# Optimization experiments

Measured on AMD Instinct MI355X. Metric: run time of the kernel, lower is better.

## Reference

```python
import jax, jax.numpy as jnp
import numpy as np

DIM = 768
NUM_HEADS = 16
D_K = DIM // NUM_HEADS


def setup_inputs() -> dict:
    key = jax.random.key(0)
    ks = jax.random.split(key, 9)
    B, T = 4, 2048
    s = 1.0 / np.sqrt(DIM)
    return {
        "x": jax.random.normal(ks[0], (B, T, DIM), dtype=jnp.float32),
        "Wq": jax.random.normal(ks[1], (DIM, DIM), dtype=jnp.float32) * s,
        "bq": jnp.zeros((DIM,), dtype=jnp.float32),
        "Wk": jax.random.normal(ks[2], (DIM, DIM), dtype=jnp.float32) * s,
        "bk": jnp.zeros((DIM,), dtype=jnp.float32),
        "Wv": jax.random.normal(ks[3], (DIM, DIM), dtype=jnp.float32) * s,
        "bv": jnp.zeros((DIM,), dtype=jnp.float32),
        "Wp": jax.random.normal(ks[4], (DIM, DIM), dtype=jnp.float32) * s,
        "bp": jnp.zeros((DIM,), dtype=jnp.float32),
    }


def reference(x, Wq, bq, Wk, bk, Wv, bv, Wp, bp):
    B, T, _ = x.shape
    # QKV projections (weights stored as [in, out])
    q = x @ Wq + bq
    k = x @ Wk + bk
    v = x @ Wv + bv
    # split heads: (B, H, T, d_k)
    q = q.reshape(B, T, NUM_HEADS, D_K).transpose(0, 2, 1, 3)
    k = k.reshape(B, T, NUM_HEADS, D_K).transpose(0, 2, 1, 3)
    v = v.reshape(B, T, NUM_HEADS, D_K).transpose(0, 2, 1, 3)
    # scaled dot-product attention; dropout omitted (eval mode)
    scores = jnp.einsum("bhtd,bhsd->bhts", q, k) / jnp.sqrt(jnp.float32(D_K))
    attn = jax.nn.softmax(scores, axis=-1)
    out = jnp.einsum("bhts,bhsd->bhtd", attn, v)
    out = out.transpose(0, 2, 1, 3).reshape(B, T, DIM)
    return out @ Wp + bp
```

## Files before the change

kernel.cpp:

```cpp
#include <hip/hip_runtime.h>
#include <math.h>

#define T_SEQ 2048
#define B_SZ  4
#define DIM   768
#define NH    16
#define DK    48
#define NQK   1536
#define N3    2304
#define LDQ   56
#define LDK   72
#define LDP   72

typedef __bf16 bf16x8 __attribute__((ext_vector_type(8)));
typedef float  f32x4  __attribute__((ext_vector_type(4)));

__device__ __forceinline__ unsigned short f32_to_bf16(float f) {
    unsigned u = __float_as_uint(f);
    u += 0x7FFFu + ((u >> 16) & 1u);
    return (unsigned short)(u >> 16);
}
__device__ __forceinline__ unsigned pack_bf16x2(float a, float b) {
    return (unsigned)f32_to_bf16(a) | ((unsigned)f32_to_bf16(b) << 16);
}
__device__ __forceinline__ void lds_dma16(const unsigned short* g, unsigned short* l) {
    __builtin_amdgcn_global_load_lds(
        (const __attribute__((address_space(1))) unsigned int*)g,
        (__attribute__((address_space(3))) unsigned int*)l, 16, 0, 0);
}

__global__ __launch_bounds__(256) void cvt_x_kernel(
    const float* __restrict__ x, unsigned short* __restrict__ xb)
{
    int i = blockIdx.x * 256 + threadIdx.x;
    const float* p = x + (size_t)i * 8;
    float4 f0 = *(const float4*)p;
    float4 f1 = *(const float4*)(p + 4);
    uint4 u;
    u.x = pack_bf16x2(f0.x, f0.y);
    u.y = pack_bf16x2(f0.z, f0.w);
    u.z = pack_bf16x2(f1.x, f1.y);
    u.w = pack_bf16x2(f1.z, f1.w);
    *(uint4*)(xb + (size_t)i * 8) = u;
}

__global__ __launch_bounds__(256) void pack_w_kernel(
    const float* __restrict__ Wq, const float* __restrict__ Wk,
    const float* __restrict__ Wv, const float* __restrict__ Wp,
    unsigned short* __restrict__ Wt, unsigned short* __restrict__ Wpt,
    float qscale)
{
    __shared__ float T[32][33];
    const int mode = blockIdx.z;
    const float* W = (mode == 0) ? Wq : (mode == 1) ? Wk : (mode == 2) ? Wv : Wp;
    const float sc = (mode == 0) ? qscale : 1.0f;
    const int k0 = blockIdx.x * 32, c0 = blockIdx.y * 32;
    const int tx = threadIdx.x & 31, ty = threadIdx.x >> 5;

#pragma unroll
    for (int r = 0; r < 4; ++r) {
        int row = ty + r * 8;
        T[row][tx] = W[(size_t)(k0 + row) * DIM + c0 + tx];
    }
    __syncthreads();
#pragma unroll
    for (int r = 0; r < 4; ++r) {
        int j   = ty + r * 8;
        int col = c0 + j;
        int k   = k0 + tx;
        unsigned short v = f32_to_bf16(T[tx][j] * sc);
        if (mode < 3) Wt[(size_t)(mode * 768 + col) * DIM + k] = v;
        else          Wpt[(size_t)col * DIM + k] = v;
    }
}

__global__ __launch_bounds__(256) void pack_bias_kernel(
    const float* __restrict__ bq, const float* __restrict__ bk,
    const float* __restrict__ bv, float* __restrict__ b3, float qscale)
{
    int n = blockIdx.x * 256 + threadIdx.x;
    if (n >= N3) return;
    float v;
    if (n < 768)       v = bq[n] * qscale;
    else if (n < 1536) v = bk[n - 768];
    else               v = bv[n - 1536];
    b3[n] = v;
}

__global__ __launch_bounds__(256, 4) void gemm_qkv_kernel(
    const unsigned short* __restrict__ A, const unsigned short* __restrict__ Bt,
    const float* __restrict__ bias, unsigned short* __restrict__ QK,
    unsigned short* __restrict__ vT)
{
    __shared__ unsigned short As[128 * 32];
    __shared__ unsigned short Bs[128 * 32];

    const int t = threadIdx.x;
    const int w = t >> 6, lane = t & 63, quad = lane >> 4, lr = lane & 15;
    const int wm = w >> 1, wn = w & 1;
    const int m0 = blockIdx.y * 128, n0 = blockIdx.x * 128;

    const int cw0 = w * 128, cw1 = w * 128 + 64;
    const int ca = cw0 + lane, cb = cw1 + lane;
    const int ra = ca >> 2, sa = (ca & 3) * 8;
    const int rb = cb >> 2, sb = (cb & 3) * 8;

    f32x4 acc[4][4] = {};

    for (int k0 = 0; k0 < DIM; k0 += 32) {
        __syncthreads();
        lds_dma16(A  + (size_t)(m0 + ra) * DIM + k0 + sa, As + cw0 * 8);
        lds_dma16(A  + (size_t)(m0 + rb) * DIM + k0 + sb, As + cw1 * 8);
        lds_dma16(Bt + (size_t)(n0 + ra) * DIM + k0 + sa, Bs + cw0 * 8);
        lds_dma16(Bt + (size_t)(n0 + rb) * DIM + k0 + sb, Bs + cw1 * 8);
        __syncthreads();

        bf16x8 af[4], bfr[4];
#pragma unroll
        for (int mt = 0; mt < 4; ++mt)
            af[mt] = *(const bf16x8*)&As[(wm * 64 + mt * 16 + lr) * 32 + quad * 8];
#pragma unroll
        for (int nt = 0; nt < 4; ++nt)
            bfr[nt] = *(const bf16x8*)&Bs[(wn * 64 + nt * 16 + lr) * 32 + quad * 8];
#pragma unroll
        for (int mt = 0; mt < 4; ++mt)
#pragma unroll
            for (int nt = 0; nt < 4; ++nt)
                acc[mt][nt] = __builtin_amdgcn_mfma_f32_16x16x32_bf16(
                    af[mt], bfr[nt], acc[mt][nt], 0, 0, 0);
    }

    if (blockIdx.x < 12) {
#pragma unroll
        for (int nt = 0; nt < 4; ++nt) {
            int col = n0 + wn * 64 + nt * 16 + lr;
            float bv = bias[col];
#pragma unroll
            for (int mt = 0; mt < 4; ++mt)
#pragma unroll
                for (int r = 0; r < 4; ++r) {
                    int row = m0 + wm * 64 + mt * 16 + quad * 4 + r;
                    QK[(size_t)row * NQK + col] = f32_to_bf16(acc[mt][nt][r] + bv);
                }
        }
    } else {
        const int bidx = m0 >> 11;
        const int ts_base = (m0 & 2047) + wm * 64;
#pragma unroll
        for (int nt = 0; nt < 4; ++nt) {
            int col = n0 + wn * 64 + nt * 16 + lr;
            int vcol = col - 1536;
            int hh = vcol / 48, cc = vcol - hh * 48;
            float bv = bias[col];
            unsigned short* dst0 = vT + ((size_t)(bidx * 16 + hh) * 48 + cc) * T_SEQ;
#pragma unroll
            for (int mt = 0; mt < 4; ++mt) {
                int ts = ts_base + mt * 16 + quad * 4;
                uint2 u;
                u.x = pack_bf16x2(acc[mt][nt][0] + bv, acc[mt][nt][1] + bv);
                u.y = pack_bf16x2(acc[mt][nt][2] + bv, acc[mt][nt][3] + bv);
                *(uint2*)(dst0 + ts) = u;
            }
        }
    }
}

__global__ __launch_bounds__(256, 4) void gemm_out_kernel(
    const unsigned short* __restrict__ A, const unsigned short* __restrict__ Bt,
    const float* __restrict__ bias, float* __restrict__ C)
{
    __shared__ unsigned short As[128 * 32];
    __shared__ unsigned short Bs[128 * 32];

    const int t = threadIdx.x;
    const int w = t >> 6, lane = t & 63, quad = lane >> 4, lr = lane & 15;
    const int wm = w >> 1, wn = w & 1;
    const int m0 = blockIdx.y * 128, n0 = blockIdx.x * 128;

    const int cw0 = w * 128, cw1 = w * 128 + 64;
    const int ca = cw0 + lane, cb = cw1 + lane;
    const int ra = ca >> 2, sa = (ca & 3) * 8;
    const int rb = cb >> 2, sb = (cb & 3) * 8;

    f32x4 acc[4][4] = {};

    for (int k0 = 0; k0 < DIM; k0 += 32) {
        __syncthreads();
        lds_dma16(A  + (size_t)(m0 + ra) * DIM + k0 + sa, As + cw0 * 8);
        lds_dma16(A  + (size_t)(m0 + rb) * DIM + k0 + sb, As + cw1 * 8);
        lds_dma16(Bt + (size_t)(n0 + ra) * DIM + k0 + sa, Bs + cw0 * 8);
        lds_dma16(Bt + (size_t)(n0 + rb) * DIM + k0 + sb, Bs + cw1 * 8);
        __syncthreads();

        bf16x8 af[4], bfr[4];
#pragma unroll
        for (int mt = 0; mt < 4; ++mt)
            af[mt] = *(const bf16x8*)&As[(wm * 64 + mt * 16 + lr) * 32 + quad * 8];
#pragma unroll
        for (int nt = 0; nt < 4; ++nt)
            bfr[nt] = *(const bf16x8*)&Bs[(wn * 64 + nt * 16 + lr) * 32 + quad * 8];
#pragma unroll
        for (int mt = 0; mt < 4; ++mt)
#pragma unroll
            for (int nt = 0; nt < 4; ++nt)
                acc[mt][nt] = __builtin_amdgcn_mfma_f32_16x16x32_bf16(
                    af[mt], bfr[nt], acc[mt][nt], 0, 0, 0);
    }

#pragma unroll
    for (int nt = 0; nt < 4; ++nt) {
        int col = n0 + wn * 64 + nt * 16 + lr;
        float bv = bias[col];
#pragma unroll
        for (int mt = 0; mt < 4; ++mt)
#pragma unroll
            for (int r = 0; r < 4; ++r) {
                int row = m0 + wm * 64 + mt * 16 + quad * 4 + r;
                C[(size_t)row * DIM + col] = acc[mt][nt][r] + bv;
            }
    }
}

__global__ __launch_bounds__(512, 6) void attn_kernel(
    const unsigned short* __restrict__ QK, const unsigned short* __restrict__ vT,
    unsigned short* __restrict__ Ob)
{
    __shared__ unsigned short smem[128 * LDQ + 64 * LDK + 64 * LDK + 8 * 16 * LDP];
    unsigned short* Qs = smem;
    unsigned short* Ks = smem + 128 * LDQ;
    unsigned short* Vt = Ks + 64 * LDK;
    unsigned short* Ps = Vt + 64 * LDK;

    const int t = threadIdx.x;
    const int w = t >> 6, lane = t & 63, quad = lane >> 4, lr = lane & 15;
    const int qt = blockIdx.x, h = blockIdx.y, b = blockIdx.z;
    const int base = b * T_SEQ, q0 = qt * 128;
    const int hq = h * DK;
    const int hk = 768 + h * DK;

    {
        int r = t / 6, c = t - r * 6;
        *(uint4*)&Qs[r * LDQ + c * 8] =
            *(const uint4*)(QK + (size_t)(base + q0 + r) * NQK + hq + c * 8);
        if (t < 256) {
            int qc2 = t + 512;
            int r2 = qc2 / 6, c2 = qc2 - r2 * 6;
            *(uint4*)&Qs[r2 * LDQ + c2 * 8] =
                *(const uint4*)(QK + (size_t)(base + q0 + r2) * NQK + hq + c2 * 8);
        }
    }
    if (t < 256) {
        int r = t >> 2, c = 48 + (t & 3) * 4;
        *(uint2*)&Ks[r * LDK + c] = make_uint2(0u, 0u);
        int vr = 48 + (t >> 4), vc = (t & 15) * 4;
        unsigned ones = (vr == 48) ? 0x3F803F80u : 0u;
        *(uint2*)&Vt[vr * LDK + vc] = make_uint2(ones, ones);
    }

    f32x4 Oacc[4] = {};
    const unsigned short* vbase = vT + (size_t)(b * 16 + h) * 48 * T_SEQ;

    for (int kt = 0; kt < T_SEQ / 64; ++kt) {
        __syncthreads();
        if (t < 384) {
            int r = t / 6, c = t - r * 6;
            *(uint4*)&Ks[r * LDK + c * 8] =
                *(const uint4*)(QK + (size_t)(base + kt * 64 + r) * NQK + hk + c * 8);
        } else {
            int vc_ = t - 384;
            int d = vc_ >> 3, ch = vc_ & 7;
            *(uint4*)&Vt[d * LDK + ch * 8] =
                *(const uint4*)(vbase + (size_t)d * T_SEQ + kt * 64 + ch * 8);
        }
        if (t < 256) {
            int vc_ = 128 + t;
            int d = vc_ >> 3, ch = vc_ & 7;
            *(uint4*)&Vt[d * LDK + ch * 8] =
                *(const uint4*)(vbase + (size_t)d * T_SEQ + kt * 64 + ch * 8);
        }
        __syncthreads();

        f32x4 S[4] = {};
        bf16x8 aQ0 = *(const bf16x8*)&Qs[(w * 16 + lr) * LDQ + quad * 8];
        bf16x8 aQ1 = *(const bf16x8*)&Qs[(w * 16 + lr) * LDQ + 32 + quad * 8];
#pragma unroll
        for (int nt = 0; nt < 4; ++nt) {
            bf16x8 b0 = *(const bf16x8*)&Ks[(nt * 16 + lr) * LDK + quad * 8];
            bf16x8 b1 = *(const bf16x8*)&Ks[(nt * 16 + lr) * LDK + 32 + quad * 8];
            S[nt] = __builtin_amdgcn_mfma_f32_16x16x32_bf16(aQ0, b0, S[nt], 0, 0, 0);
            S[nt] = __builtin_amdgcn_mfma_f32_16x16x32_bf16(aQ1, b1, S[nt], 0, 0, 0);
        }

        unsigned short* Pw = Ps + w * 16 * LDP;
#pragma unroll
        for (int nt = 0; nt < 4; ++nt)
#pragma unroll
            for (int r = 0; r < 4; ++r)
                Pw[(quad * 4 + r) * LDP + nt * 16 + lr] =
                    f32_to_bf16(__builtin_amdgcn_exp2f(S[nt][r]));

        bf16x8 aP0 = *(const bf16x8*)&Pw[lr * LDP + quad * 8];
        bf16x8 aP1 = *(const bf16x8*)&Pw[lr * LDP + 32 + quad * 8];
#pragma unroll
        for (int on = 0; on < 4; ++on) {
            bf16x8 b0 = *(const bf16x8*)&Vt[(on * 16 + lr) * LDK + quad * 8];
            bf16x8 b1 = *(const bf16x8*)&Vt[(on * 16 + lr) * LDK + 32 + quad * 8];
            Oacc[on] = __builtin_amdgcn_mfma_f32_16x16x32_bf16(aP0, b0, Oacc[on], 0, 0, 0);
            Oacc[on] = __builtin_amdgcn_mfma_f32_16x16x32_bf16(aP1, b1, Oacc[on], 0, 0, 0);
        }
    }

#pragma unroll
    for (int r = 0; r < 4; ++r) {
        float l = __shfl(Oacc[3][r], lane & 0x30);
        float inv = 1.0f / l;
        int row = base + q0 + w * 16 + quad * 4 + r;
#pragma unroll
        for (int on = 0; on < 3; ++on)
            Ob[(size_t)row * DIM + h * DK + on * 16 + lr] =
                f32_to_bf16(Oacc[on][r] * inv);
    }
}

extern "C" void kernel_launch(void* const* d_in, const int* in_sizes, int n_in,
                              void* d_out, int out_size, void* d_ws, size_t ws_size,
                              hipStream_t stream) {
    (void)in_sizes; (void)n_in; (void)out_size; (void)ws_size;

    const float* x  = (const float*)d_in[0];
    const float* Wq = (const float*)d_in[1];
    const float* bq = (const float*)d_in[2];
    const float* Wk = (const float*)d_in[3];
    const float* bk = (const float*)d_in[4];
    const float* Wv = (const float*)d_in[5];
    const float* bv = (const float*)d_in[6];
    const float* Wp = (const float*)d_in[7];
    const float* bp = (const float*)d_in[8];
    float* out = (float*)d_out;

    const size_t M = (size_t)B_SZ * T_SEQ;

    char* ws = (char*)d_ws;
    unsigned short* xb  = (unsigned short*)ws;  ws += M * DIM * 2;
    unsigned short* qk  = (unsigned short*)ws;  ws += M * NQK * 2;
    unsigned short* vT  = (unsigned short*)ws;  ws += M * DIM * 2;
    unsigned short* aob = (unsigned short*)ws;  ws += M * DIM * 2;
    unsigned short* Wt  = (unsigned short*)ws;  ws += (size_t)N3 * DIM * 2;
    unsigned short* Wpt = (unsigned short*)ws;  ws += (size_t)DIM * DIM * 2;
    float*          b3  = (float*)ws;           ws += N3 * 4;

    const float qscale = 0.14433756729740643f * 1.4426950408889634f;

    cvt_x_kernel<<<dim3((int)(M * DIM / 8 / 256)), 256, 0, stream>>>(x, xb);
    pack_w_kernel<<<dim3(DIM / 32, DIM / 32, 4), 256, 0, stream>>>(
        Wq, Wk, Wv, Wp, Wt, Wpt, qscale);
    pack_bias_kernel<<<dim3((N3 + 255) / 256), 256, 0, stream>>>(bq, bk, bv, b3, qscale);

    gemm_qkv_kernel<<<dim3(N3 / 128, (int)(M / 128)), 256, 0, stream>>>(
        xb, Wt, b3, qk, vT);

    attn_kernel<<<dim3(T_SEQ / 128, NH, B_SZ), 512, 0, stream>>>(qk, vT, aob);

    gemm_out_kernel<<<dim3(DIM / 128, (int)(M / 128)), 256, 0, stream>>>(
        aob, Wpt, bp, out);
}
```

Before: 295.9 us.

## Restructure attention to load K/V fragments directly from global, drop shared staging

The attention kernel now runs 256 threads per block, each wave owning 32 query rows. Q, K and V MFMA fragments are read straight from global memory (relying on L1/L2), so the shared-memory K/V tiles and their per-iteration barriers go away. S is computed transposed (K as A operand), and the softmax row sum is accumulated with shuffles instead of an appended ones column in V. Shared memory now holds only the per-wave P buffer. The trade is redundant global/cache traffic for K/V across waves in exchange for no block-level sync. Launch-bounds occupancy hints on the GEMMs are also relaxed.

After: 361.6 us. +22.2%, slower.

```diff
diff --git a/kernel.cpp b/kernel.cpp
--- a/kernel.cpp
+++ b/kernel.cpp
@@ -8,9 +8,7 @@
 #define DK    48
 #define NQK   1536
 #define N3    2304
-#define LDQ   56
-#define LDK   72
-#define LDP   72
+#define LDP   64
 
 typedef __bf16 bf16x8 __attribute__((ext_vector_type(8)));
 typedef float  f32x4  __attribute__((ext_vector_type(4)));
@@ -87,7 +85,7 @@
     b3[n] = v;
 }
 
-__global__ __launch_bounds__(256, 4) void gemm_qkv_kernel(
+__global__ __launch_bounds__(256) void gemm_qkv_kernel(
     const unsigned short* __restrict__ A, const unsigned short* __restrict__ Bt,
     const float* __restrict__ bias, unsigned short* __restrict__ QK,
     unsigned short* __restrict__ vT)
@@ -165,7 +163,7 @@
     }
 }
 
-__global__ __launch_bounds__(256, 4) void gemm_out_kernel(
+__global__ __launch_bounds__(256) void gemm_out_kernel(
     const unsigned short* __restrict__ A, const unsigned short* __restrict__ Bt,
     const float* __restrict__ bias, float* __restrict__ C)
 {
@@ -221,104 +219,101 @@
     }
 }
 
-__global__ __launch_bounds__(512, 6) void attn_kernel(
+__global__ __launch_bounds__(256, 4) void attn_kernel(
     const unsigned short* __restrict__ QK, const unsigned short* __restrict__ vT,
     unsigned short* __restrict__ Ob)
 {
-    __shared__ unsigned short smem[128 * LDQ + 64 * LDK + 64 * LDK + 8 * 16 * LDP];
-    unsigned short* Qs = smem;
-    unsigned short* Ks = smem + 128 * LDQ;
-    unsigned short* Vt = Ks + 64 * LDK;
-    unsigned short* Ps = Vt + 64 * LDK;
+    __shared__ unsigned short Ps[128 * LDP];
 
     const int t = threadIdx.x;
     const int w = t >> 6, lane = t & 63, quad = lane >> 4, lr = lane & 15;
     const int qt = blockIdx.x, h = blockIdx.y, b = blockIdx.z;
     const int base = b * T_SEQ, q0 = qt * 128;
-    const int hq = h * DK;
-    const int hk = 768 + h * DK;
-
-    {
-        int r = t / 6, c = t - r * 6;
-        *(uint4*)&Qs[r * LDQ + c * 8] =
-            *(const uint4*)(QK + (size_t)(base + q0 + r) * NQK + hq + c * 8);
-        if (t < 256) {
-            int qc2 = t + 512;
-            int r2 = qc2 / 6, c2 = qc2 - r2 * 6;
-            *(uint4*)&Qs[r2 * LDQ + c2 * 8] =
-                *(const uint4*)(QK + (size_t)(base + q0 + r2) * NQK + hq + c2 * 8);
-        }
-    }
-    if (t < 256) {
-        int r = t >> 2, c = 48 + (t & 3) * 4;
-        *(uint2*)&Ks[r * LDK + c] = make_uint2(0u, 0u);
-        int vr = 48 + (t >> 4), vc = (t & 15) * 4;
-        unsigned ones = (vr == 48) ? 0x3F803F80u : 0u;
-        *(uint2*)&Vt[vr * LDK + vc] = make_uint2(ones, ones);
-    }
-
-    f32x4 Oacc[4] = {};
-    const unsigned short* vbase = vT + (size_t)(b * 16 + h) * 48 * T_SEQ;
+    const int hq = h * DK, hk = 768 + h * DK;
+    const int qrow = base + q0 + w * 32;
+
+    bf16x8 qa[2], qb[2];
+#pragma unroll
+    for (int mt = 0; mt < 2; ++mt) {
+        const unsigned short* qp = QK + (size_t)(qrow + mt * 16 + lr) * NQK + hq;
+        qa[mt] = *(const bf16x8*)(qp + quad * 8);
+        qb[mt] = *(const bf16x8*)(qp + 32 + quad * 8);
+    }
+
+    f32x4 Oacc[2][3] = {};
+    float l_acc[2] = {0.0f, 0.0f};
+    const unsigned short* vbase = vT + (size_t)(b * NH + h) * DK * T_SEQ;
+    unsigned short* Pw = Ps + (w * 32) * LDP;
+    const bf16x8 zfrag = {};
 
     for (int kt = 0; kt < T_SEQ / 64; ++kt) {
-        __syncthreads();
-        if (t < 384) {
-            int r = t / 6, c = t - r * 6;
-            *(uint4*)&Ks[r * LDK + c * 8] =
-                *(const uint4*)(QK + (size_t)(base + kt * 64 + r) * NQK + hk + c * 8);
-        } else {
-            int vc_ = t - 384;
-            int d = vc_ >> 3, ch = vc_ & 7;
-            *(uint4*)&Vt[d * LDK + ch * 8] =
-                *(const uint4*)(vbase + (size_t)d * T_SEQ + kt * 64 + ch * 8);
-        }
-        if (t < 256) {
-            int vc_ = 128 + t;
-            int d = vc_ >> 3, ch = vc_ & 7;
-            *(uint4*)&Vt[d * LDK + ch * 8] =
-                *(const uint4*)(vbase + (size_t)d * T_SEQ + kt * 64 + ch * 8);
-        }
-        __syncthreads();
-
-        f32x4 S[4] = {};
-        bf16x8 aQ0 = *(const bf16x8*)&Qs[(w * 16 + lr) * LDQ + quad * 8];
-        bf16x8 aQ1 = *(const bf16x8*)&Qs[(w * 16 + lr) * LDQ + 32 + quad * 8];
+        bf16x8 ka[4], kb[4];
 #pragma unroll
         for (int nt = 0; nt < 4; ++nt) {
-            bf16x8 b0 = *(const bf16x8*)&Ks[(nt * 16 + lr) * LDK + quad * 8];
-            bf16x8 b1 = *(const bf16x8*)&Ks[(nt * 16 + lr) * LDK + 32 + quad * 8];
-            S[nt] = __builtin_amdgcn_mfma_f32_16x16x32_bf16(aQ0, b0, S[nt], 0, 0, 0);
-            S[nt] = __builtin_amdgcn_mfma_f32_16x16x32_bf16(aQ1, b1, S[nt], 0, 0, 0);
-        }
-
-        unsigned short* Pw = Ps + w * 16 * LDP;
-#pragma unroll
-        for (int nt = 0; nt < 4; ++nt)
-#pragma unroll
-            for (int r = 0; r < 4; ++r)
-                Pw[(quad * 4 + r) * LDP + nt * 16 + lr] =
-                    f32_to_bf16(__builtin_amdgcn_exp2f(S[nt][r]));
-
-        bf16x8 aP0 = *(const bf16x8*)&Pw[lr * LDP + quad * 8];
-        bf16x8 aP1 = *(const bf16x8*)&Pw[lr * LDP + 32 + quad * 8];
-#pragma unroll
-        for (int on = 0; on < 4; ++on) {
-            bf16x8 b0 = *(const bf16x8*)&Vt[(on * 16 + lr) * LDK + quad * 8];
-            bf16x8 b1 = *(const bf16x8*)&Vt[(on * 16 + lr) * LDK + 32 + quad * 8];
-            Oacc[on] = __builtin_amdgcn_mfma_f32_16x16x32_bf16(aP0, b0, Oacc[on], 0, 0, 0);
-            Oacc[on] = __builtin_amdgcn_mfma_f32_16x16x32_bf16(aP1, b1, Oacc[on], 0, 0, 0);
-        }
-    }
-
-#pragma unroll
-    for (int r = 0; r < 4; ++r) {
-        float l = __shfl(Oacc[3][r], lane & 0x30);
-        float inv = 1.0f / l;
-        int row = base + q0 + w * 16 + quad * 4 + r;
-#pragma unroll
-        for (int on = 0; on < 3; ++on)
-            Ob[(size_t)row * DIM + h * DK + on * 16 + lr] =
-                f32_to_bf16(Oacc[on][r] * inv);
+            const unsigned short* kp =
+                QK + (size_t)(base + kt * 64 + nt * 16 + lr) * NQK + hk;
+            ka[nt] = *(const bf16x8*)(kp + quad * 8);
+            kb[nt] = (quad < 2) ? *(const bf16x8*)(kp + 32 + quad * 8) : zfrag;
+        }
+
+#pragma unroll
+        for (int mt = 0; mt < 2; ++mt) {
+            float rs = 0.0f;
+#pragma unroll
+            for (int nt = 0; nt < 4; ++nt) {
+                f32x4 st = {};
+                st = __builtin_amdgcn_mfma_f32_16x16x32_bf16(ka[nt], qa[mt], st, 0, 0, 0);
+                st = __builtin_amdgcn_mfma_f32_16x16x32_bf16(kb[nt], qb[mt], st, 0, 0, 0);
+                float p0 = __builtin_amdgcn_exp2f(st[0]);
+                float p1 = __builtin_amdgcn_exp2f(st[1]);
+                float p2 = __builtin_amdgcn_exp2f(st[2]);
+                float p3 = __builtin_amdgcn_exp2f(st[3]);
+                rs += (p0 + p1) + (p2 + p3);
+                uint2 pk;
+                pk.x = pack_bf16x2(p0, p1);
+                pk.y = pack_bf16x2(p2, p3);
+                *(uint2*)&Pw[(mt * 16 + lr) * LDP + nt * 16 + quad * 4] = pk;
+            }
+            rs += __shfl_xor(rs, 16);
+            rs += __shfl_xor(rs, 32);
+            l_acc[mt] += rs;
+        }
+
+        bf16x8 aP[2][2];
+#pragma unroll
+        for (int mt = 0; mt < 2; ++mt) {
+            aP[mt][0] = *(const bf16x8*)&Pw[(mt * 16 + lr) * LDP + quad * 8];
+            aP[mt][1] = *(const bf16x8*)&Pw[(mt * 16 + lr) * LDP + 32 + quad * 8];
+        }
+
+#pragma unroll
+        for (int on = 0; on < 3; ++on) {
+            const unsigned short* vp =
+                vbase + (size_t)(on * 16 + lr) * T_SEQ + kt * 64;
+            bf16x8 v0 = *(const bf16x8*)(vp + quad * 8);
+            bf16x8 v1 = *(const bf16x8*)(vp + 32 + quad * 8);
+#pragma unroll
+            for (int mt = 0; mt < 2; ++mt) {
+                Oacc[mt][on] = __builtin_amdgcn_mfma_f32_16x16x32_bf16(
+                    aP[mt][0], v0, Oacc[mt][on], 0, 0, 0);
+                Oacc[mt][on] = __builtin_amdgcn_mfma_f32_16x16x32_bf16(
+                    aP[mt][1], v1, Oacc[mt][on], 0, 0, 0);
+            }
+        }
+    }
+
+#pragma unroll
+    for (int mt = 0; mt < 2; ++mt) {
+#pragma unroll
+        for (int r = 0; r < 4; ++r) {
+            float l = __shfl(l_acc[mt], quad * 4 + r);
+            float inv = 1.0f / l;
+            int row = qrow + mt * 16 + quad * 4 + r;
+#pragma unroll
+            for (int on = 0; on < 3; ++on)
+                Ob[(size_t)row * DIM + h * DK + on * 16 + lr] =
+                    f32_to_bf16(Oacc[mt][on][r] * inv);
+        }
     }
 }
 
@@ -359,7 +354,7 @@
     gemm_qkv_kernel<<<dim3(N3 / 128, (int)(M / 128)), 256, 0, stream>>>(
         xb, Wt, b3, qk, vT);
 
-    attn_kernel<<<dim3(T_SEQ / 128, NH, B_SZ), 512, 0, stream>>>(qk, vT, aob);
+    attn_kernel<<<dim3(T_SEQ / 128, NH, B_SZ), 256, 0, stream>>>(qk, vT, aob);
 
     gemm_out_kernel<<<dim3(DIM / 128, (int)(M / 128)), 256, 0, stream>>>(
         aob, Wpt, bp, out);
```
